# Optimization experiments

Hardware: AMD Instinct MI355X
Metric: run time of the kernel (lower is better)

## Reference

```python
import jax, jax.numpy as jnp
import numpy as np

N_HEADS = 16


def setup_inputs() -> dict:
    key = jax.random.key(0)
    k1, k2 = jax.random.split(key)
    B, S, D = 2, 2048, 2048
    x = jax.random.normal(k1, (B, S, D), dtype=jnp.float32)
    # torch nn.Linear(dim, 3*dim): y = x @ W^T + b; store W in jax layout [D, 3D]
    W_qkv = jax.random.normal(k2, (D, 3 * D), dtype=jnp.float32) * (D ** -0.5)
    b_qkv = jnp.zeros((3 * D,), dtype=jnp.float32)
    mask = jnp.ones((B, S), dtype=bool)
    return {"x": x, "W_qkv": W_qkv, "b_qkv": b_qkv, "mask": mask}


def reference(x, W_qkv, b_qkv, mask):
    B, S, D = x.shape
    H = N_HEADS
    hd = D // H
    scale = hd ** -0.5
    qkv = x @ W_qkv + b_qkv                      # [B,S,3D]
    q, k, v = jnp.split(qkv, 3, axis=-1)
    # [B,S,D] -> [B,H,S,hd]
    reshape = lambda t: t.reshape(B, S, H, hd).transpose(0, 2, 1, 3)
    q, k, v = reshape(q), reshape(k), reshape(v)
    sim = jnp.einsum('bhqd,bhkd->bhqk', q, k) * scale   # [B,H,S,S]
    neg = -jnp.finfo(sim.dtype).max
    sim = jnp.where(mask[:, None, None, :], sim, neg)   # padding mask on keys
    attn = jax.nn.softmax(sim, axis=-1)
    out = jnp.einsum('bhqk,bhkd->bhqd', attn, v)        # [B,H,S,hd]
    return out.transpose(0, 2, 1, 3).reshape(B, S, D)
```

## Files before the change

### kernel.cpp

```cpp
#include <hip/hip_runtime.h>
#include <hip/hip_bf16.h>
#include <math.h>

typedef __attribute__((ext_vector_type(8))) short bf16x8;
typedef __attribute__((ext_vector_type(4))) float f32x4;
typedef __attribute__((ext_vector_type(16))) float f32x16;
typedef __attribute__((ext_vector_type(4))) short short4v;
typedef __attribute__((ext_vector_type(4))) int int4v;

__device__ __forceinline__ short f2bf(float f) {
  union { float f; unsigned u; } v; v.f = f;
  unsigned r = v.u + 0x7fffu + ((v.u >> 16) & 1u);
  return (short)(r >> 16);
}

__device__ __forceinline__ unsigned cvt_pk_bf16(float lo, float hi) {
  unsigned r;
  asm volatile("v_cvt_pk_bf16_f32 %0, %1, %2" : "=v"(r) : "v"(lo), "v"(hi));
  return r;
}


__global__ void convert_x_kernel(const float* __restrict__ x, short* __restrict__ xb, int n) {
  int i = (blockIdx.x * blockDim.x + threadIdx.x) * 4;
  int stride = gridDim.x * blockDim.x * 4;
  for (; i < n; i += stride) {
    float4 v = *(const float4*)(x + i);
    short4v o;
    o.x = f2bf(v.x); o.y = f2bf(v.y); o.z = f2bf(v.z); o.w = f2bf(v.w);
    *(short4v*)(xb + i) = o;
  }
}

__global__ void transpose_w_kernel(const float* __restrict__ W, short* __restrict__ Wt) {
  __shared__ short tile[32][33];
  int n0 = blockIdx.x * 32, k0 = blockIdx.y * 32;
  int tx = threadIdx.x, ty = threadIdx.y;
#pragma unroll
  for (int u = 0; u < 4; ++u) {
    int k = k0 + ty + u * 8;
    tile[ty + u * 8][tx] = f2bf(W[(size_t)k * 6144 + n0 + tx]);
  }
  __syncthreads();
#pragma unroll
  for (int u = 0; u < 4; ++u) {
    int n = n0 + ty + u * 8;
    Wt[(size_t)n * 2048 + k0 + tx] = tile[tx][ty + u * 8];
  }
}

__global__ void mask_norm_kernel(const unsigned* __restrict__ m, unsigned char* __restrict__ out, int n) {
  __shared__ int flagA, flagB;
  if (threadIdx.x == 0) { flagA = 0; flagB = 0; }
  __syncthreads();
  int a = 0, b = 0;
  for (int i = threadIdx.x; i < n / 4; i += blockDim.x) {
    unsigned wv = m[i];
    if (wv > 1u) a = 1;
    if (wv != 0u && wv != 0x3f800000u) b = 1;
  }
  if (a) atomicOr(&flagA, 1);
  if (b) atomicOr(&flagB, 1);
  __syncthreads();
  int A = flagA, B = flagB;
  for (int i = threadIdx.x; i < n; i += blockDim.x) {
    unsigned char r;
    if (!A) r = (m[i] != 0u) ? 1 : 0;
    else if (!B) r = (((const float*)m)[i] != 0.f) ? 1 : 0;
    else r = (((const unsigned char*)m)[i] != 0) ? 1 : 0;
    out[i] = r;
  }
}


__global__ __launch_bounds__(256, 3) void qkv_gemm_kernel(
    const short* __restrict__ A, const short* __restrict__ Bt, const float* __restrict__ bias,
    short* __restrict__ qws, short* __restrict__ kws, short* __restrict__ vtws) {
  __shared__ __align__(16) char smem[17408];
  short* As = (short*)smem;
  short* Bs = (short*)(smem + 8192);
  short* Vs = (short*)smem;

  const int K = 2048;
  int lid = blockIdx.x;
  int swz = (lid & 7) * 192 + (lid >> 3);
  int tm = swz / 48, tn = swz % 48;
  int m0 = tm * 128, n0 = tn * 128;
  int t = threadIdx.x, lane = t & 63, w = t >> 6;
  int wr = w >> 1, wc = w & 1;
  int g = lane >> 4, c = lane & 15;

  f32x4 acc[4][4] = {};

  for (int k0 = 0; k0 < K; k0 += 32) {
#pragma unroll
    for (int rep = 0; rep < 2; ++rep) {
      int chunk = rep * 256 + t;
      int row = chunk >> 2, cc = chunk & 3;
      const short* ga = A + (size_t)(m0 + row) * K + (k0 + cc * 8);
      __builtin_amdgcn_global_load_lds((const __attribute__((address_space(1))) void*)ga,
          (__attribute__((address_space(3))) void*)(As + chunk * 8), 16, 0, 0);
      const short* gb = Bt + (size_t)(n0 + row) * K + (k0 + cc * 8);
      __builtin_amdgcn_global_load_lds((const __attribute__((address_space(1))) void*)gb,
          (__attribute__((address_space(3))) void*)(Bs + chunk * 8), 16, 0, 0);
    }
    __syncthreads();
    bf16x8 ar[4], br[4];
#pragma unroll
    for (int i = 0; i < 4; ++i) ar[i] = *(const bf16x8*)(As + (wr * 64 + i * 16 + c) * 32 + g * 8);
#pragma unroll
    for (int j = 0; j < 4; ++j) br[j] = *(const bf16x8*)(Bs + (wc * 64 + j * 16 + c) * 32 + g * 8);
#pragma unroll
    for (int i = 0; i < 4; ++i)
#pragma unroll
      for (int j = 0; j < 4; ++j)
        acc[i][j] = __builtin_amdgcn_mfma_f32_16x16x32_bf16(ar[i], br[j], acc[i][j], 0, 0, 0);
    __syncthreads();
  }

  int sec = n0 >> 11;
  int h = (n0 >> 7) & 15;
  int b = m0 >> 11;
  int s0 = m0 & 2047;
  size_t bh = (size_t)(b * 16 + h);

  if (sec < 2) {
    short* dst = (sec == 0 ? qws : kws) + bh * (size_t)(2048 * 128);
    const float sc = (sec == 0) ? (0.08838834764831845f * 1.4426950408889634f) : 1.0f;
#pragma unroll
    for (int i = 0; i < 4; ++i)
#pragma unroll
      for (int j = 0; j < 4; ++j) {
        int dcol = wc * 64 + j * 16 + c;
        float bv = bias[n0 + dcol];
#pragma unroll
        for (int r = 0; r < 4; ++r) {
          int srow = s0 + wr * 64 + i * 16 + g * 4 + r;
          dst[(size_t)srow * 128 + dcol] = f2bf((acc[i][j][r] + bv) * sc);
        }
      }
  } else {
    short* dst = vtws + bh * (size_t)(128 * 2048);
#pragma unroll
    for (int hs = 0; hs < 2; ++hs) {
      if (wr == hs) {
#pragma unroll
        for (int i = 0; i < 4; ++i)
#pragma unroll
          for (int j = 0; j < 4; ++j) {
            int dcol = wc * 64 + j * 16 + c;
            float bv = bias[n0 + dcol];
#pragma unroll
            for (int r = 0; r < 4; ++r)
              Vs[(i * 16 + g * 4 + r) * 136 + dcol] = f2bf(acc[i][j][r] + bv);
          }
      }
      __syncthreads();
      {
        int d = t >> 1, sc2 = (t & 1) * 32;
        size_t off = (size_t)d * 2048 + s0 + hs * 64 + sc2;
#pragma unroll
        for (int q = 0; q < 4; ++q) {
          int4v pk;
#pragma unroll
          for (int e = 0; e < 4; ++e) {
            int u = q * 8 + e * 2;
            unsigned lo = (unsigned short)Vs[(sc2 + u) * 136 + d];
            unsigned hi = (unsigned short)Vs[(sc2 + u + 1) * 136 + d];
            pk[e] = (int)(lo | (hi << 16));
          }
          ((int4v*)(dst + off))[q] = pk;
        }
      }
      __syncthreads();
    }
  }
}


__global__ __launch_bounds__(256, 2) void attn_kernel(
    const short* __restrict__ qws, const short* __restrict__ kws, const short* __restrict__ vtws,
    const unsigned char* __restrict__ maskb, float* __restrict__ out) {
  __shared__ short Ks[2][32 * 128];
  __shared__ short Vs[2][128 * 32];
  __shared__ short P[4][32 * 40];
  __shared__ float biasLds[2048];
  __shared__ int flagsLds[64];

  const int S = 2048, HD = 128;
  int lid = blockIdx.x;
  int swz = (lid & 7) * 64 + (lid >> 3);
  int bh = swz >> 4, qblk = swz & 15;
  int b = bh >> 4, h = bh & 15;
  int t = threadIdx.x, lane = t & 63, w = t >> 6;
  int ql = lane & 31, hi = lane >> 5;
  int q0 = qblk * 128 + w * 32;
  const short* Q = qws + (size_t)bh * S * HD;
  const short* Kp = kws + (size_t)bh * S * HD;
  const short* Vt = vtws + (size_t)bh * HD * S;
  const unsigned char* mk = maskb + b * S;
  const float NEG = -3.4028235e38f;

#define STAGE_KV(buf, kv0_)                                                              \
  {                                                                                      \
    _Pragma("unroll")                                                                    \
    for (int rr = 0; rr < 2; ++rr) {                                                     \
      int ci = rr * 256 + t;                                                             \
      int r = ci >> 4, cin = ci & 15;                                                    \
      const short* gk = Kp + (size_t)((kv0_) + r) * HD + ((cin ^ (r & 7)) * 8);          \
      __builtin_amdgcn_global_load_lds((const __attribute__((address_space(1))) void*)gk,\
          (__attribute__((address_space(3))) void*)(&Ks[buf][0] + ci * 8), 16, 0, 0);    \
    }                                                                                    \
    _Pragma("unroll")                                                                    \
    for (int rr = 0; rr < 2; ++rr) {                                                     \
      int ci = rr * 256 + t;                                                             \
      int r = ci >> 2, cin = ci & 3;                                                     \
      const short* gv = Vt + (size_t)r * S + (kv0_) + ((cin ^ ((r >> 1) & 3)) * 8);      \
      __builtin_amdgcn_global_load_lds((const __attribute__((address_space(1))) void*)gv,\
          (__attribute__((address_space(3))) void*)(&Vs[buf][0] + ci * 8), 16, 0, 0);    \
    }                                                                                    \
  }

  bf16x8 qf[8];
#pragma unroll
  for (int kc = 0; kc < 8; ++kc)
    qf[kc] = *(const bf16x8*)(Q + (size_t)(q0 + ql) * HD + kc * 16 + hi * 8);

  for (int i = t; i < 2048; i += 256) biasLds[i] = mk[i] ? 0.f : NEG;
  STAGE_KV(0, 0);
  __syncthreads();
  if (t < 64) {
    int ok = 1;
    for (int j = 0; j < 32; ++j) ok &= (biasLds[t * 32 + j] == 0.f) ? 1 : 0;
    flagsLds[t] = ok;
  }
  __syncthreads();

  f32x16 acc[4] = {};
  float m_ = NEG, lp = 0.f;
  short* pl = &P[w][0];
  int cur = 0;

  for (int it = 0; it < 64; ++it) {
    int kv0 = it * 32;
    if (it + 1 < 64) STAGE_KV(cur ^ 1, kv0 + 32);

    const short* ks = &Ks[cur][0];
    const short* vs = &Vs[cur][0];

    f32x16 sv = {};
    __builtin_amdgcn_s_setprio(1);
#pragma unroll
    for (int kc = 0; kc < 8; ++kc) {
      int chunk = (kc * 2 + hi) ^ (ql & 7);
      bf16x8 kf = *(const bf16x8*)(ks + ql * 128 + chunk * 8);
      sv = __builtin_amdgcn_mfma_f32_32x32x16_bf16(kf, qf[kc], sv, 0, 0, 0);
    }
    __builtin_amdgcn_s_setprio(0);

    float p[16];
    int fl = flagsLds[it];
    if (fl) {
#pragma unroll
      for (int r = 0; r < 16; ++r) p[r] = sv[r];
    } else {
#pragma unroll
      for (int g2 = 0; g2 < 4; ++g2) {
        f32x4 bb = *(const f32x4*)(biasLds + kv0 + g2 * 8 + hi * 4);
#pragma unroll
        for (int j = 0; j < 4; ++j) p[g2 * 4 + j] = sv[g2 * 4 + j] + bb[j];
      }
    }

    float a0 = fmaxf(fmaxf(p[0], p[1]), fmaxf(p[2], p[3]));
    float a1 = fmaxf(fmaxf(p[4], p[5]), fmaxf(p[6], p[7]));
    float a2 = fmaxf(fmaxf(p[8], p[9]), fmaxf(p[10], p[11]));
    float a3 = fmaxf(fmaxf(p[12], p[13]), fmaxf(p[14], p[15]));
    float rmx = fmaxf(fmaxf(a0, a1), fmaxf(a2, a3));
    rmx = fmaxf(rmx, __shfl_xor(rmx, 32));

    if (__any(rmx > m_ + 12.f)) {
      float mn = fmaxf(m_, rmx);
      float al = exp2f(m_ - mn);
      m_ = mn; lp *= al;
#pragma unroll
      for (int dt = 0; dt < 4; ++dt)
#pragma unroll
        for (int r = 0; r < 16; ++r) acc[dt][r] *= al;
    }

    float e[16];
#pragma unroll
    for (int r = 0; r < 16; ++r) e[r] = exp2f(p[r] - m_);
    float s0 = ((e[0] + e[1]) + (e[2] + e[3])) + ((e[4] + e[5]) + (e[6] + e[7]));
    float s1 = ((e[8] + e[9]) + (e[10] + e[11])) + ((e[12] + e[13]) + (e[14] + e[15]));
    lp += s0 + s1;

#pragma unroll
    for (int g2 = 0; g2 < 4; ++g2) {
      int2 pk;
      pk.x = (int)cvt_pk_bf16(e[4 * g2 + 0], e[4 * g2 + 1]);
      pk.y = (int)cvt_pk_bf16(e[4 * g2 + 2], e[4 * g2 + 3]);
      *(int2*)(pl + ql * 40 + g2 * 8 + hi * 4) = pk;
    }

    bf16x8 pf[2];
#pragma unroll
    for (int kt = 0; kt < 2; ++kt)
      pf[kt] = *(const bf16x8*)(pl + ql * 40 + (kt * 2 + hi) * 8);

    __builtin_amdgcn_s_setprio(1);
#pragma unroll
    for (int dt = 0; dt < 4; ++dt) {
      int d = dt * 32 + ql;
#pragma unroll
      for (int kt = 0; kt < 2; ++kt) {
        int chunk = (kt * 2 + hi) ^ ((d >> 1) & 3);
        bf16x8 vf = *(const bf16x8*)(vs + d * 32 + chunk * 8);
        acc[dt] = __builtin_amdgcn_mfma_f32_32x32x16_bf16(vf, pf[kt], acc[dt], 0, 0, 0);
      }
    }
    __builtin_amdgcn_s_setprio(0);

    __syncthreads();
    cur ^= 1;
  }

  lp += __shfl_xor(lp, 32);
  float inv = 1.f / lp;
  size_t orow = (size_t)(b * 2048 + q0 + ql) * 2048 + h * 128;
#pragma unroll
  for (int dt = 0; dt < 4; ++dt)
#pragma unroll
    for (int g2 = 0; g2 < 4; ++g2) {
      f32x4 v;
      v[0] = acc[dt][g2 * 4 + 0] * inv;
      v[1] = acc[dt][g2 * 4 + 1] * inv;
      v[2] = acc[dt][g2 * 4 + 2] * inv;
      v[3] = acc[dt][g2 * 4 + 3] * inv;
      int d = dt * 32 + g2 * 8 + hi * 4;
      *(f32x4*)(out + orow + d) = v;
    }
#undef STAGE_KV
}


extern "C" void kernel_launch(void* const* d_in, const int* in_sizes, int n_in,
                              void* d_out, int out_size, void* d_ws, size_t ws_size,
                              hipStream_t stream) {
  const float* x = (const float*)d_in[0];
  const float* W = (const float*)d_in[1];
  const float* bias = (const float*)d_in[2];
  const void* mask = d_in[3];
  float* out = (float*)d_out;

  char* ws = (char*)d_ws;
  short* xb = (short*)(ws);
  short* wt = (short*)(ws + 16777216);
  short* qws = (short*)(ws + 41943040);
  short* kws = (short*)(ws + 58720256);
  short* vtws = (short*)(ws + 75497472);
  unsigned char* maskb = (unsigned char*)(ws + 92274688);

  convert_x_kernel<<<dim3(2048), dim3(256), 0, stream>>>(x, xb, 2 * 2048 * 2048);
  transpose_w_kernel<<<dim3(192, 64), dim3(32, 8), 0, stream>>>(W, wt);
  mask_norm_kernel<<<dim3(1), dim3(256), 0, stream>>>((const unsigned*)mask, maskb, 2 * 2048);
  qkv_gemm_kernel<<<dim3(1536), dim3(256), 0, stream>>>(xb, wt, bias, qws, kws, vtws);
  attn_kernel<<<dim3(512), dim3(256), 0, stream>>>(qws, kws, vtws, maskb, out);
}
```

Baseline: 373.5 us.

## Rewrite QKV GEMM with 256x256 tiles, double-buffered swizzled LDS pipeline

The QKV projection GEMM moves from 128x128 tiles with four waves and a single LDS buffer to 256x256 tiles with eight waves. It now double-buffers 64-wide K slices through XOR-swizzled LDS, interleaves async global-to-LDS loads with MFMA quarters, and raises wave priority around the MFMA blocks. The V-transpose epilogue is redone per wave in swizzled LDS with 16-byte stores. The aim is more reuse per tile and hiding of load latency behind compute. The cost is a 128 KB LDS footprint, which limits each CU to one block, and a 384-block grid that may leave a partial wave at the tail.

After: 350.0 us. 6.3% less time.

```diff
diff --git a/kernel.cpp b/kernel.cpp
--- a/kernel.cpp
+++ b/kernel.cpp
@@ -73,108 +73,159 @@
 }
 
 
-__global__ __launch_bounds__(256, 3) void qkv_gemm_kernel(
+__global__ __launch_bounds__(512, 2) void qkv_gemm_kernel(
     const short* __restrict__ A, const short* __restrict__ Bt, const float* __restrict__ bias,
     short* __restrict__ qws, short* __restrict__ kws, short* __restrict__ vtws) {
-  __shared__ __align__(16) char smem[17408];
-  short* As = (short*)smem;
-  short* Bs = (short*)(smem + 8192);
-  short* Vs = (short*)smem;
-
-  const int K = 2048;
+  __shared__ __align__(16) char smem[131072];
+
   int lid = blockIdx.x;
-  int swz = (lid & 7) * 192 + (lid >> 3);
-  int tm = swz / 48, tn = swz % 48;
-  int m0 = tm * 128, n0 = tn * 128;
+  int swz = (lid & 7) * 48 + (lid >> 3);
+  int tm = swz / 24, tn = swz % 24;
+  int m0 = tm * 256, n0 = tn * 256;
   int t = threadIdx.x, lane = t & 63, w = t >> 6;
-  int wr = w >> 1, wc = w & 1;
+  int wr = w >> 2, wc = w & 3;
   int g = lane >> 4, c = lane & 15;
 
-  f32x4 acc[4][4] = {};
-
-  for (int k0 = 0; k0 < K; k0 += 32) {
-#pragma unroll
-    for (int rep = 0; rep < 2; ++rep) {
-      int chunk = rep * 256 + t;
-      int row = chunk >> 2, cc = chunk & 3;
-      const short* ga = A + (size_t)(m0 + row) * K + (k0 + cc * 8);
-      __builtin_amdgcn_global_load_lds((const __attribute__((address_space(1))) void*)ga,
-          (__attribute__((address_space(3))) void*)(As + chunk * 8), 16, 0, 0);
-      const short* gb = Bt + (size_t)(n0 + row) * K + (k0 + cc * 8);
-      __builtin_amdgcn_global_load_lds((const __attribute__((address_space(1))) void*)gb,
-          (__attribute__((address_space(3))) void*)(Bs + chunk * 8), 16, 0, 0);
-    }
-    __syncthreads();
-    bf16x8 ar[4], br[4];
-#pragma unroll
-    for (int i = 0; i < 4; ++i) ar[i] = *(const bf16x8*)(As + (wr * 64 + i * 16 + c) * 32 + g * 8);
-#pragma unroll
-    for (int j = 0; j < 4; ++j) br[j] = *(const bf16x8*)(Bs + (wc * 64 + j * 16 + c) * 32 + g * 8);
-#pragma unroll
-    for (int i = 0; i < 4; ++i)
-#pragma unroll
-      for (int j = 0; j < 4; ++j)
-        acc[i][j] = __builtin_amdgcn_mfma_f32_16x16x32_bf16(ar[i], br[j], acc[i][j], 0, 0, 0);
-    __syncthreads();
+#define AHP(P, hm) (smem + (P) * 65536 + (hm) * 16384)
+#define BHP(P, hn) (smem + (P) * 65536 + 32768 + (hn) * 16384)
+
+#define STAGE_HALF(ldsb, gbase)                                                            \
+  { _Pragma("unroll")                                                                      \
+    for (int rr = 0; rr < 2; ++rr) {                                                       \
+      int ci = rr * 512 + t;                                                               \
+      int row_ = ci >> 3, ch_ = ci & 7;                                                    \
+      const short* gp_ = (gbase) + (size_t)row_ * 2048 + ((ch_ ^ (row_ & 7)) * 8);         \
+      __builtin_amdgcn_global_load_lds((const __attribute__((address_space(1))) void*)gp_, \
+          (__attribute__((address_space(3))) void*)((ldsb) + ci * 16), 16, 0, 0);          \
+    } }
+
+#define LD_A(half)                                                                          \
+  { const char* ab_ = AHP(P, half);                                                         \
+    _Pragma("unroll")                                                                       \
+    for (int mi = 0; mi < 4; ++mi) {                                                        \
+      int row_ = wr * 16 + c + mi * 32;                                                     \
+      _Pragma("unroll")                                                                     \
+      for (int ks = 0; ks < 2; ++ks)                                                        \
+        af[mi][ks] = *(const bf16x8*)(ab_ + row_ * 128 + (((ks * 4 + g) ^ (row_ & 7)) * 16)); \
+    } }
+#define LD_B(half)                                                                          \
+  { const char* bb_ = BHP(P, half);                                                         \
+    _Pragma("unroll")                                                                       \
+    for (int nj = 0; nj < 2; ++nj) {                                                        \
+      int row_ = wc * 16 + c + nj * 64;                                                     \
+      _Pragma("unroll")                                                                     \
+      for (int ks = 0; ks < 2; ++ks)                                                        \
+        bfr[nj][ks] = *(const bf16x8*)(bb_ + row_ * 128 + (((ks * 4 + g) ^ (row_ & 7)) * 16)); \
+    } }
+#define MFMA16(MI0, NJ0)                                                                    \
+  __builtin_amdgcn_s_setprio(1);                                                            \
+  _Pragma("unroll")                                                                         \
+  for (int mi = 0; mi < 4; ++mi)                                                            \
+    _Pragma("unroll")                                                                       \
+    for (int nj = 0; nj < 2; ++nj)                                                          \
+      _Pragma("unroll")                                                                     \
+      for (int ks = 0; ks < 2; ++ks)                                                        \
+        acc[(MI0) + mi][(NJ0) + nj] =                                                       \
+            __builtin_amdgcn_mfma_f32_16x16x32_bf16(af[mi][ks], bfr[nj][ks],                \
+                                                    acc[(MI0) + mi][(NJ0) + nj], 0, 0, 0);  \
+  __builtin_amdgcn_s_setprio(0);
+
+  STAGE_HALF(AHP(0, 0), A + (size_t)m0 * 2048);
+  STAGE_HALF(BHP(0, 0), Bt + (size_t)n0 * 2048);
+  STAGE_HALF(BHP(0, 1), Bt + (size_t)(n0 + 128) * 2048);
+  STAGE_HALF(AHP(0, 1), A + (size_t)(m0 + 128) * 2048);
+  asm volatile("s_waitcnt vmcnt(4)" ::: "memory");
+  __builtin_amdgcn_s_barrier();
+
+  f32x4 acc[8][4] = {};
+
+  for (int tk = 0; tk < 32; ++tk) {
+    int P = tk & 1, Pn = P ^ 1;
+    bool pf = (tk + 1 < 32);
+    int k1 = (tk + 1) * 64;
+    bf16x8 af[4][2], bfr[2][2];
+
+    LD_A(0); LD_B(0);
+    if (pf) STAGE_HALF(AHP(Pn, 0), A + (size_t)m0 * 2048 + k1);
+    MFMA16(0, 0);
+    if (pf) { asm volatile("s_waitcnt vmcnt(4)" ::: "memory"); }
+    else    { asm volatile("s_waitcnt vmcnt(2)" ::: "memory"); }
+    __builtin_amdgcn_s_barrier();
+
+    LD_B(1);
+    if (pf) STAGE_HALF(BHP(Pn, 0), Bt + (size_t)n0 * 2048 + k1);
+    MFMA16(0, 2);
+    if (pf) { asm volatile("s_waitcnt vmcnt(4)" ::: "memory"); }
+    else    { asm volatile("s_waitcnt vmcnt(0)" ::: "memory"); }
+    __builtin_amdgcn_s_barrier();
+
+    LD_A(1);
+    if (pf) STAGE_HALF(BHP(Pn, 1), Bt + (size_t)(n0 + 128) * 2048 + k1);
+    MFMA16(4, 2);
+    __builtin_amdgcn_s_barrier();
+
+    LD_B(0);
+    if (pf) STAGE_HALF(AHP(Pn, 1), A + (size_t)(m0 + 128) * 2048 + k1);
+    MFMA16(4, 0);
+    if (pf) { asm volatile("s_waitcnt vmcnt(4)" ::: "memory"); }
+    __builtin_amdgcn_s_barrier();
   }
 
   int sec = n0 >> 11;
-  int h = (n0 >> 7) & 15;
   int b = m0 >> 11;
   int s0 = m0 & 2047;
-  size_t bh = (size_t)(b * 16 + h);
+  int nsec = n0 & 2047;
 
   if (sec < 2) {
-    short* dst = (sec == 0 ? qws : kws) + bh * (size_t)(2048 * 128);
-    const float sc = (sec == 0) ? (0.08838834764831845f * 1.4426950408889634f) : 1.0f;
-#pragma unroll
-    for (int i = 0; i < 4; ++i)
-#pragma unroll
-      for (int j = 0; j < 4; ++j) {
-        int dcol = wc * 64 + j * 16 + c;
-        float bv = bias[n0 + dcol];
+    short* base = (sec == 0 ? qws : kws);
+    const float scq = (sec == 0) ? (0.08838834764831845f * 1.4426950408889634f) : 1.0f;
+#pragma unroll
+    for (int nj = 0; nj < 4; ++nj) {
+      int colsec = nsec + wc * 16 + nj * 64;
+      float bv = bias[n0 + wc * 16 + nj * 64 + c];
+      int h = colsec >> 7;
+      int d = (colsec & 127) + c;
+      short* dst = base + ((size_t)(b * 16 + h)) * (2048 * 128) + d;
+#pragma unroll
+      for (int mi = 0; mi < 8; ++mi) {
+        int srow = s0 + (wr + 2 * mi) * 16 + g * 4;
+#pragma unroll
+        for (int r = 0; r < 4; ++r)
+          dst[(size_t)(srow + r) * 128] = f2bf((acc[mi][nj][r] + bv) * scq);
+      }
+    }
+  } else {
+    __builtin_amdgcn_s_barrier();
+    char* wreg = smem + w * 16384;
+#pragma unroll
+    for (int nj = 0; nj < 4; ++nj) {
+      float bv = bias[n0 + wc * 16 + nj * 64 + c];
+      int d = nj * 16 + c;
+#pragma unroll
+      for (int mi = 0; mi < 8; ++mi)
 #pragma unroll
         for (int r = 0; r < 4; ++r) {
-          int srow = s0 + wr * 64 + i * 16 + g * 4 + r;
-          dst[(size_t)srow * 128 + dcol] = f2bf((acc[i][j][r] + bv) * sc);
+          int sloc = mi * 16 + g * 4 + r;
+          *(short*)(wreg + d * 256 + (((sloc >> 3) ^ (d & 15)) * 16) + (sloc & 7) * 2) =
+              f2bf(acc[mi][nj][r] + bv);
         }
-      }
-  } else {
-    short* dst = vtws + bh * (size_t)(128 * 2048);
-#pragma unroll
-    for (int hs = 0; hs < 2; ++hs) {
-      if (wr == hs) {
-#pragma unroll
-        for (int i = 0; i < 4; ++i)
-#pragma unroll
-          for (int j = 0; j < 4; ++j) {
-            int dcol = wc * 64 + j * 16 + c;
-            float bv = bias[n0 + dcol];
-#pragma unroll
-            for (int r = 0; r < 4; ++r)
-              Vs[(i * 16 + g * 4 + r) * 136 + dcol] = f2bf(acc[i][j][r] + bv);
-          }
-      }
-      __syncthreads();
-      {
-        int d = t >> 1, sc2 = (t & 1) * 32;
-        size_t off = (size_t)d * 2048 + s0 + hs * 64 + sc2;
-#pragma unroll
-        for (int q = 0; q < 4; ++q) {
-          int4v pk;
-#pragma unroll
-          for (int e = 0; e < 4; ++e) {
-            int u = q * 8 + e * 2;
-            unsigned lo = (unsigned short)Vs[(sc2 + u) * 136 + d];
-            unsigned hi = (unsigned short)Vs[(sc2 + u + 1) * 136 + d];
-            pk[e] = (int)(lo | (hi << 16));
-          }
-          ((int4v*)(dst + off))[q] = pk;
-        }
-      }
-      __syncthreads();
-    }
-  }
+    }
+#pragma unroll
+    for (int q = 0; q < 16; ++q) {
+      int d = q * 4 + g;
+      bf16x8 v = *(const bf16x8*)(wreg + d * 256 + ((c ^ (d & 15)) * 16));
+      int colsec = nsec + wc * 16 + (d >> 4) * 64 + (d & 15);
+      int h = colsec >> 7, dloc = colsec & 127;
+      int srow = s0 + wr * 16 + (c >> 1) * 32 + (c & 1) * 8;
+      *(bf16x8*)(vtws + ((size_t)(b * 16 + h)) * (128 * 2048) + (size_t)dloc * 2048 + srow) = v;
+    }
+  }
+#undef AHP
+#undef BHP
+#undef STAGE_HALF
+#undef LD_A
+#undef LD_B
+#undef MFMA16
 }
 
 
@@ -365,6 +416,6 @@
   convert_x_kernel<<<dim3(2048), dim3(256), 0, stream>>>(x, xb, 2 * 2048 * 2048);
   transpose_w_kernel<<<dim3(192, 64), dim3(32, 8), 0, stream>>>(W, wt);
   mask_norm_kernel<<<dim3(1), dim3(256), 0, stream>>>((const unsigned*)mask, maskb, 2 * 2048);
-  qkv_gemm_kernel<<<dim3(1536), dim3(256), 0, stream>>>(xb, wt, bias, qws, kws, vtws);
+  qkv_gemm_kernel<<<dim3(384), dim3(512), 0, stream>>>(xb, wt, bias, qws, kws, vtws);
   attn_kernel<<<dim3(512), dim3(256), 0, stream>>>(qws, kws, vtws, maskb, out);
 }
```
